# Performance work log

Hardware: AMD Instinct MI355X
Metric: run time of the kernel (lower is better)

Reference implementation:

```python
import jax, jax.numpy as jnp
import numpy as np

B, C, Q, E, H = 8, 1024, 128, 512, 1024


def setup_inputs() -> dict:
    key = jax.random.key(0)
    ks = jax.random.split(key, 8)
    return {
        "context": jax.random.normal(ks[0], (B, C, E), jnp.float32),
        "question": jax.random.normal(ks[1], (B, Q, E), jnp.float32),
        "context_mask": jnp.ones((B, C), jnp.float32),
        "w_question": jax.random.normal(ks[2], (E,), jnp.float32),
        "w_context": jax.random.normal(ks[3], (E,), jnp.float32),
        "w_multiple": jax.random.normal(ks[4], (E,), jnp.float32),
        "W1": jax.random.normal(ks[5], (4 * E, H), jnp.float32) * 0.02,
        "b1": jnp.zeros((H,), jnp.float32),
        "W2": jax.random.normal(ks[6], (H, 4 * E), jnp.float32) * 0.02,
        "b2": jnp.zeros((4 * E,), jnp.float32),
    }


def reference(context, question, context_mask, w_question, w_context, w_multiple, W1, b1, W2, b2):
    # Dropout is identity at eval time.
    # Trilinear similarity: s[b,c,q] = q.w_q + ctx.w_c + sum_e q_e*ctx_e*w_m_e
    q_w = question @ w_question                                  # (B,Q)
    c_w = context @ w_context                                    # (B,C)
    mult = jnp.einsum("bqe,bce->bcq", question * w_multiple, context)  # avoids (B,C,Q,E)
    sim = q_w[:, None, :] + c_w[:, :, None] + mult               # (B,C,Q)

    # Context2Query: softmax over question dim (dim=2)
    c2q = jnp.einsum("bcq,bqe->bce", jax.nn.softmax(sim, axis=2), question)
    # Query2Context: max over question dim, softmax over context dim (dim=1)
    q2c = jnp.einsum("bc,bce->be", jax.nn.softmax(jnp.max(sim, axis=2), axis=1), context)  # (B,E)

    attended = jnp.concatenate(
        [context, c2q, context * c2q, context * q2c[:, None, :]], axis=2
    )  # (B,C,4E)

    # MaskedLinear: linear then zero out masked context positions
    m = context_mask[:, :, None]
    h = (attended @ W1 + b1) * m
    out = jax.nn.relu((h @ W2 + b2) * m)
    return out
```

## Files before the change

### kernel.cpp

```cpp
#include <hip/hip_runtime.h>

typedef __bf16 bf16;
typedef __bf16 bf16x2 __attribute__((ext_vector_type(2)));
typedef __bf16 bf16x4 __attribute__((ext_vector_type(4)));
typedef __bf16 bf16x8 __attribute__((ext_vector_type(8)));
typedef float f32x4 __attribute__((ext_vector_type(4)));

#define AS1 __attribute__((address_space(1)))
#define AS3 __attribute__((address_space(3)))

__device__ __forceinline__ void async_copy16(const void* g, void* l) {
  __builtin_amdgcn_global_load_lds((const AS1 void*)g, (AS3 void*)l, 16, 0, 0);
}

#define BB 8
#define CC 1024
#define QQ 128
#define EE 512
#define HH 1024
#define FOURE 2048

__global__ __launch_bounds__(256) void prep_kernel(
    const float* __restrict__ W1, const float* __restrict__ W2,
    const float* __restrict__ qst, const float* __restrict__ wmul,
    const float* __restrict__ wqv, bf16* __restrict__ W1T,
    bf16* __restrict__ W2T, bf16* __restrict__ qT,
    bf16* __restrict__ qmh, bf16* __restrict__ qml, float* __restrict__ qw) {
  __shared__ float tile[32][33];
  __shared__ float r4[4];
  int bx = blockIdx.x;
  int t = threadIdx.x;
  if (bx >= 4608) {
    int i = bx - 4608;
    int half = t >> 7, tr = t & 127;
    int rowg = i * 2 + half;
    const float* qrow = qst + (size_t)rowg * EE;
    float4 qv = *(const float4*)&qrow[tr * 4];
    float4 wm4 = *(const float4*)&wmul[tr * 4];
    float4 wq4 = *(const float4*)&wqv[tr * 4];
    float m[4] = {qv.x * wm4.x, qv.y * wm4.y, qv.z * wm4.z, qv.w * wm4.w};
    bf16x4 h, l;
#pragma unroll
    for (int k = 0; k < 4; ++k) {
      bf16 hh = (bf16)m[k];
      h[k] = hh; l[k] = (bf16)(m[k] - (float)hh);
    }
    *(bf16x4*)&qmh[(size_t)rowg * EE + tr * 4] = h;
    *(bf16x4*)&qml[(size_t)rowg * EE + tr * 4] = l;
    float s = qv.x * wq4.x + qv.y * wq4.y + qv.z * wq4.z + qv.w * wq4.w;
#pragma unroll
    for (int off = 32; off; off >>= 1) s += __shfl_xor(s, off);
    if ((t & 63) == 0) r4[t >> 6] = s;
    __syncthreads();
    if (tr == 0) qw[rowg] = r4[half * 2] + r4[half * 2 + 1];
    return;
  }
  const float* src;
  bf16* dst;
  int R, C, idx;
  if (bx < 2048) {
    src = W1; dst = W1T; R = 2048; C = 1024; idx = bx;
  } else if (bx < 4096) {
    src = W2; dst = W2T; R = 1024; C = 2048; idx = bx - 2048;
  } else {
    int i = bx - 4096;
    int b = i >> 6; idx = i & 63;
    src = qst + (size_t)b * QQ * EE; dst = qT + (size_t)b * EE * QQ;
    R = 128; C = 512;
  }
  int ctiles = C >> 5;
  int by = idx / ctiles, cx = idx % ctiles;
  int tx = t & 31, ty = t >> 5;
#pragma unroll
  for (int rr = 0; rr < 4; ++rr)
    tile[ty + rr * 8][tx] = src[(size_t)(by * 32 + ty + rr * 8) * C + cx * 32 + tx];
  __syncthreads();
#pragma unroll
  for (int rr = 0; rr < 4; ++rr)
    dst[(size_t)(cx * 32 + ty + rr * 8) * R + by * 32 + tx] = (bf16)tile[tx][ty + rr * 8];
}

__global__ __launch_bounds__(256) void fused_att_kernel(
    const float* __restrict__ ctx, const bf16* __restrict__ qmh,
    const bf16* __restrict__ qml, const bf16* __restrict__ qT,
    const float* __restrict__ wc, const float* __restrict__ qw,
    float* __restrict__ smax, bf16* __restrict__ att) {
  int b = blockIdx.y;
  int m0 = blockIdx.x * 16;
  __shared__ __align__(16) char U[26880];
  bf16* Ah = (bf16*)(U);
  bf16* Al = (bf16*)(U + 1024);
  bf16* Bh = (bf16*)(U + 2048);
  bf16* Bl = (bf16*)(U + 10240);
  float(*sim_s)[132] = (float(*)[132])(U + 18432);
  bf16* c2q_lds = (bf16*)(U);
  __shared__ float wc_s[EE];
  __shared__ float qw_s[QQ];
  __shared__ float cw_s[16];
  __shared__ bf16 P_lds[16][136];
  int t = threadIdx.x;
  for (int i = t; i < EE; i += 256) wc_s[i] = wc[i];
  if (t < QQ) qw_s[t] = qw[b * QQ + t];
  __syncthreads();
  int wv = t >> 6, ln = t & 63;
  int rl = ln & 15, kq = ln >> 4;
  f32x4 acc[2] = {};
  const float* Ag = ctx + ((size_t)b * CC + m0) * EE;
  const bf16* Bhg = qmh + (size_t)b * QQ * EE;
  const bf16* Blg = qml + (size_t)b * QQ * EE;
  int arow = t >> 4, ae = (t & 15) * 2;
  float cwp = 0.f;
  for (int k0 = 0; k0 < EE; k0 += 32) {
    {
      float2 v = *(const float2*)(Ag + (size_t)arow * EE + k0 + ae);
      cwp += v.x * wc_s[k0 + ae] + v.y * wc_s[k0 + ae + 1];
      bf16 h0 = (bf16)v.x, h1 = (bf16)v.y;
      bf16x2 h, l;
      h[0] = h0; h[1] = h1;
      l[0] = (bf16)(v.x - (float)h0);
      l[1] = (bf16)(v.y - (float)h1);
      int sl = ((ae >> 3) ^ ((arow >> 1) & 3)) * 8 + (ae & 7);
      *(bf16x2*)&Ah[arow * 32 + sl] = h;
      *(bf16x2*)&Al[arow * 32 + sl] = l;
    }
#pragma unroll
    for (int r = 0; r < 2; ++r) {
      int fb = (r * 4 + wv) * 1024 + ln * 16;
      int row = fb >> 6;
      int cq = ((fb >> 4) & 3) ^ ((row >> 1) & 3);
      async_copy16(Bhg + (size_t)row * EE + k0 + cq * 8, (char*)Bh + fb);
      async_copy16(Blg + (size_t)row * EE + k0 + cq * 8, (char*)Bl + fb);
    }
    __syncthreads();
    bf16x8 ah, al, bh[2], bl[2];
    {
      int sl = (kq ^ ((rl >> 1) & 3)) * 8;
      ah = *(const bf16x8*)&Ah[rl * 32 + sl];
      al = *(const bf16x8*)&Al[rl * 32 + sl];
    }
#pragma unroll
    for (int j = 0; j < 2; ++j) {
      int r = wv * 32 + j * 16 + rl;
      int sl = (kq ^ ((r >> 1) & 3)) * 8;
      bh[j] = *(const bf16x8*)&Bh[r * 32 + sl];
      bl[j] = *(const bf16x8*)&Bl[r * 32 + sl];
    }
#pragma unroll
    for (int j = 0; j < 2; ++j) {
      acc[j] = __builtin_amdgcn_mfma_f32_16x16x32_bf16(ah, bh[j], acc[j], 0, 0, 0);
      acc[j] = __builtin_amdgcn_mfma_f32_16x16x32_bf16(ah, bl[j], acc[j], 0, 0, 0);
      acc[j] = __builtin_amdgcn_mfma_f32_16x16x32_bf16(al, bh[j], acc[j], 0, 0, 0);
    }
    __syncthreads();
  }
  {
    float s = cwp;
    s += __shfl_xor(s, 1); s += __shfl_xor(s, 2);
    s += __shfl_xor(s, 4); s += __shfl_xor(s, 8);
    if ((t & 15) == 0) cw_s[arow] = s;
  }
#pragma unroll
  for (int j = 0; j < 2; ++j) {
    int col = wv * 32 + j * 16 + rl;
    float qv = qw_s[col];
    int rbase = kq * 4;
#pragma unroll
    for (int r = 0; r < 4; ++r) sim_s[rbase + r][col] = acc[j][r] + qv;
  }
  __syncthreads();
  {
    int row = t >> 4, cb = t & 15;
    float v[8];
    float mx = -3.4e38f;
#pragma unroll
    for (int k = 0; k < 8; ++k) {
      v[k] = sim_s[row][cb + 16 * k];
      mx = fmaxf(mx, v[k]);
    }
    mx = fmaxf(mx, __shfl_xor(mx, 1));
    mx = fmaxf(mx, __shfl_xor(mx, 2));
    mx = fmaxf(mx, __shfl_xor(mx, 4));
    mx = fmaxf(mx, __shfl_xor(mx, 8));
    float sm = 0.f;
#pragma unroll
    for (int k = 0; k < 8; ++k) { v[k] = __expf(v[k] - mx); sm += v[k]; }
    sm += __shfl_xor(sm, 1);
    sm += __shfl_xor(sm, 2);
    sm += __shfl_xor(sm, 4);
    sm += __shfl_xor(sm, 8);
    float inv = 1.0f / sm;
#pragma unroll
    for (int k = 0; k < 8; ++k) P_lds[row][cb + 16 * k] = (bf16)(v[k] * inv);
    if (cb == 0) smax[b * CC + m0 + row] = mx + cw_s[row];
  }
  __syncthreads();
  f32x4 acc2[8] = {};
  const bf16* qTb = qT + (size_t)b * EE * QQ;
#pragma unroll
  for (int kk = 0; kk < 4; ++kk) {
    bf16x8 af2;
    {
      bf16x4 lo = *(const bf16x4*)&P_lds[rl][kk * 32 + kq * 8];
      bf16x4 hi = *(const bf16x4*)&P_lds[rl][kk * 32 + kq * 8 + 4];
      af2[0] = lo[0]; af2[1] = lo[1]; af2[2] = lo[2]; af2[3] = lo[3];
      af2[4] = hi[0]; af2[5] = hi[1]; af2[6] = hi[2]; af2[7] = hi[3];
    }
#pragma unroll
    for (int j = 0; j < 8; ++j) {
      int n = wv * 128 + j * 16 + rl;
      bf16x8 bfr = *(const bf16x8*)&qTb[(size_t)n * QQ + kk * 32 + kq * 8];
      acc2[j] = __builtin_amdgcn_mfma_f32_16x16x32_bf16(af2, bfr, acc2[j], 0, 0, 0);
    }
  }
#pragma unroll
  for (int j = 0; j < 8; ++j) {
    int col = wv * 128 + j * 16 + rl;
    int rbase = kq * 4;
#pragma unroll
    for (int r = 0; r < 4; ++r)
      c2q_lds[(size_t)(rbase + r) * 520 + col] = (bf16)acc2[j][r];
  }
  __syncthreads();
  {
    int row = t >> 4, tc = t & 15;
    const float* crow = ctx + ((size_t)(b * CC + m0 + row)) * EE;
    bf16* arow_p = att + ((size_t)(b * CC + m0 + row)) * FOURE;
#pragma unroll
    for (int cc = 0; cc < 4; ++cc) {
      int col = cc * 128 + tc * 8;
      bf16x8 q8 = *(const bf16x8*)&c2q_lds[(size_t)row * 520 + col];
      float4 v0 = *(const float4*)&crow[col];
      float4 v1 = *(const float4*)&crow[col + 4];
      float cv[8] = {v0.x, v0.y, v0.z, v0.w, v1.x, v1.y, v1.z, v1.w};
      bf16x8 o0, o2;
#pragma unroll
      for (int k = 0; k < 8; ++k) {
        o0[k] = (bf16)cv[k];
        o2[k] = (bf16)(cv[k] * (float)q8[k]);
      }
      *(bf16x8*)&arow_p[col] = o0;
      *(bf16x8*)&arow_p[EE + col] = q8;
      *(bf16x8*)&arow_p[2 * EE + col] = o2;
    }
  }
}

__global__ __launch_bounds__(256) void q2c_kernel(
    const float* __restrict__ ctx, const float* __restrict__ smax,
    float* __restrict__ q2c) {
  int b = blockIdx.x >> 5, ch = blockIdx.x & 31;
  int t = threadIdx.x;
  __shared__ float red[256];
  __shared__ float w_s[32];
  float v[4];
  float mx = -3.4e38f;
#pragma unroll
  for (int i = 0; i < 4; ++i) {
    v[i] = smax[b * CC + i * 256 + t];
    mx = fmaxf(mx, v[i]);
  }
  red[t] = mx;
  __syncthreads();
  for (int s = 128; s > 0; s >>= 1) {
    if (t < s) red[t] = fmaxf(red[t], red[t + s]);
    __syncthreads();
  }
  mx = red[0];
  __syncthreads();
  float sm = 0.f;
#pragma unroll
  for (int i = 0; i < 4; ++i) sm += __expf(v[i] - mx);
  red[t] = sm;
  __syncthreads();
  for (int s = 128; s > 0; s >>= 1) {
    if (t < s) red[t] += red[t + s];
    __syncthreads();
  }
  float inv = 1.0f / red[0];
  if (t < 32) w_s[t] = __expf(smax[b * CC + ch * 32 + t] - mx) * inv;
  __syncthreads();
  int e = t * 2;
  const float* cb = ctx + ((size_t)b * CC + ch * 32) * EE;
  float a0 = 0.f, a1 = 0.f;
#pragma unroll 8
  for (int r = 0; r < 32; ++r) {
    float2 vv = *(const float2*)&cb[(size_t)r * EE + e];
    float w = w_s[r];
    a0 += w * vv.x;
    a1 += w * vv.y;
  }
  atomicAdd(&q2c[b * EE + e], a0);
  atomicAdd(&q2c[b * EE + e + 1], a1);
}

__global__ __launch_bounds__(256) void att3_kernel(
    const float* __restrict__ ctx, const float* __restrict__ q2c,
    bf16* __restrict__ att) {
  int idx = blockIdx.x * 256 + threadIdx.x;
  int row = idx >> 6;
  int e = (idx & 63) * 8;
  int b = row >> 10;
  float4 v0 = *(const float4*)&ctx[(size_t)row * EE + e];
  float4 v1 = *(const float4*)&ctx[(size_t)row * EE + e + 4];
  float4 g0 = *(const float4*)&q2c[b * EE + e];
  float4 g1 = *(const float4*)&q2c[b * EE + e + 4];
  bf16x8 o;
  o[0] = (bf16)(v0.x * g0.x); o[1] = (bf16)(v0.y * g0.y);
  o[2] = (bf16)(v0.z * g0.z); o[3] = (bf16)(v0.w * g0.w);
  o[4] = (bf16)(v1.x * g1.x); o[5] = (bf16)(v1.y * g1.y);
  o[6] = (bf16)(v1.z * g1.z); o[7] = (bf16)(v1.w * g1.w);
  *(bf16x8*)&att[(size_t)row * FOURE + 3 * EE + e] = o;
}

template <int OUT_BF16, int RELU>
__global__ __launch_bounds__(512, 2) void gemm_bt_db_kernel(
    const bf16* __restrict__ A, const bf16* __restrict__ Bt,
    const float* __restrict__ bias, const float* __restrict__ mask,
    void* __restrict__ Cout, int M, int N, int K) {
  __shared__ bf16 As[3][128 * 64];
  __shared__ bf16 Bs[3][256 * 64];
  int ntn = N >> 8;
  int nblk = (M >> 7) * ntn;
  int cpx = nblk >> 3;
  int bid = blockIdx.x;
  int swz = (bid & 7) * cpx + (bid >> 3);
  int mt = swz / ntn, ntb = swz - mt * ntn;
  int m0 = mt << 7, n0 = ntb << 8;
  int t = threadIdx.x, wv = t >> 6, ln = t & 63;
  int wm = wv >> 2, wn = wv & 3;
  int rl = ln & 15, kq = ln >> 4;
  int NT = K >> 6;

  auto stage = [&](int buf, int kt) {
    int k0 = kt << 6;
#pragma unroll
    for (int r = 0; r < 2; ++r) {
      int fb = r * 8192 + t * 16;
      int row = fb >> 7;
      int q = ((fb >> 4) & 7) ^ (row & 7);
      async_copy16(A + (size_t)(m0 + row) * K + k0 + q * 8,
                   (char*)As[buf] + fb);
    }
#pragma unroll
    for (int r = 0; r < 4; ++r) {
      int fb = r * 8192 + t * 16;
      int row = fb >> 7;
      int q = ((fb >> 4) & 7) ^ (row & 7);
      async_copy16(Bt + (size_t)(n0 + row) * K + k0 + q * 8,
                   (char*)Bs[buf] + fb);
    }
  };

  stage(0, 0);
  stage(1, 1);
  asm volatile("s_waitcnt vmcnt(6)" ::: "memory");
  __builtin_amdgcn_s_barrier();
  asm volatile("" ::: "memory");

  f32x4 acc[4][4] = {};
  int cur = 0, nx2 = 2;
  for (int tt = 0; tt < NT; ++tt) {
    if (tt + 2 < NT) stage(nx2, tt + 2);
    const bf16* Ab = As[cur];
    const bf16* Bb = Bs[cur];
#pragma unroll
    for (int ks = 0; ks < 2; ++ks) {
      int c = ks * 4 + kq;
      bf16x8 af[4], bfr[4];
#pragma unroll
      for (int i = 0; i < 4; ++i) {
        int row = wm * 64 + i * 16 + rl;
        af[i] = *(const bf16x8*)&Ab[row * 64 + ((c ^ (row & 7)) * 8)];
      }
#pragma unroll
      for (int j = 0; j < 4; ++j) {
        int row = wn * 64 + j * 16 + rl;
        bfr[j] = *(const bf16x8*)&Bb[row * 64 + ((c ^ (row & 7)) * 8)];
      }
#pragma unroll
      for (int i = 0; i < 4; ++i)
#pragma unroll
        for (int j = 0; j < 4; ++j)
          acc[i][j] = __builtin_amdgcn_mfma_f32_16x16x32_bf16(
              af[i], bfr[j], acc[i][j], 0, 0, 0);
    }
    if (tt + 1 < NT) {
      if (tt + 2 < NT)
        asm volatile("s_waitcnt vmcnt(6)" ::: "memory");
      else
        asm volatile("s_waitcnt vmcnt(0)" ::: "memory");
      __builtin_amdgcn_s_barrier();
      asm volatile("" ::: "memory");
    }
    cur = cur == 2 ? 0 : cur + 1;
    nx2 = nx2 == 2 ? 0 : nx2 + 1;
  }

#pragma unroll
  for (int j = 0; j < 4; ++j) {
    int col = n0 + wn * 64 + j * 16 + rl;
    float bv = bias[col];
#pragma unroll
    for (int i = 0; i < 4; ++i) {
      int rbase = m0 + wm * 64 + i * 16 + (kq << 2);
#pragma unroll
      for (int r = 0; r < 4; ++r) {
        int row = rbase + r;
        float v = acc[i][j][r] + bv;
        v *= mask[row];
        if (RELU) v = fmaxf(v, 0.f);
        if (OUT_BF16)
          ((bf16*)Cout)[(size_t)row * N + col] = (bf16)v;
        else
          ((float*)Cout)[(size_t)row * N + col] = v;
      }
    }
  }
}

extern "C" void kernel_launch(void* const* d_in, const int* in_sizes, int n_in,
                              void* d_out, int out_size, void* d_ws, size_t ws_size,
                              hipStream_t stream) {
  const float* ctx = (const float*)d_in[0];
  const float* qst = (const float*)d_in[1];
  const float* mask = (const float*)d_in[2];
  const float* wqv = (const float*)d_in[3];
  const float* wcv = (const float*)d_in[4];
  const float* wmul = (const float*)d_in[5];
  const float* W1 = (const float*)d_in[6];
  const float* b1 = (const float*)d_in[7];
  const float* W2 = (const float*)d_in[8];
  const float* b2 = (const float*)d_in[9];
  float* out = (float*)d_out;
  char* ws = (char*)d_ws;

  bf16* att = (bf16*)(ws);
  bf16* hbuf = (bf16*)(ws + 33554432);
  bf16* W1T = (bf16*)(ws + 50331648);
  bf16* W2T = (bf16*)(ws + 54525952);
  bf16* qT = (bf16*)(ws + 58720256);
  bf16* qmh = (bf16*)(ws + 59768832);
  bf16* qml = (bf16*)(ws + 60817408);
  float* smax = (float*)(ws + 61865984);
  float* q2c = (float*)(ws + 61898752);
  float* qw = (float*)(ws + 61915136);

  prep_kernel<<<5120, 256, 0, stream>>>(W1, W2, qst, wmul, wqv,
                                        W1T, W2T, qT, qmh, qml, qw);
  fused_att_kernel<<<dim3(64, BB), 256, 0, stream>>>(ctx, qmh, qml, qT, wcv,
                                                     qw, smax, att);
  hipMemsetAsync(q2c, 0, BB * EE * sizeof(float), stream);
  q2c_kernel<<<256, 256, 0, stream>>>(ctx, smax, q2c);
  att3_kernel<<<2048, 256, 0, stream>>>(ctx, q2c, att);
  gemm_bt_db_kernel<1, 0><<<256, 512, 0, stream>>>(
      att, W1T, b1, mask, hbuf, 8192, 1024, 2048);
  gemm_bt_db_kernel<0, 1><<<512, 512, 0, stream>>>(
      hbuf, W2T, b2, mask, out, 8192, 2048, 1024);
}
```

Measured before the change: 238.5 us.

## Restructure bf16 GEMM into 256x128 tiles with split-phase prefetch and MFMA priority

The two MLP GEMMs now use 256x128 block tiles with a 4x2 wave layout and a grouped block-to-tile mapping, in place of 128x256 tiles with an XCD-strided swizzle. Each K step is split into two halves. Each half reads its LDS fragments, issues part of the next-next stage's async global-to-LDS loads, and then runs its MFMAs at raised wave priority. The aim is to interleave global loads, LDS reads and matrix work across waves so more latency is hidden. The cost is more barriers per K iteration and a different L2 reuse pattern from the new tile order.

```diff
diff --git a/kernel.cpp b/kernel.cpp
--- a/kernel.cpp
+++ b/kernel.cpp
@@ -313,87 +313,115 @@
 }
 
 template <int OUT_BF16, int RELU>
-__global__ __launch_bounds__(512, 2) void gemm_bt_db_kernel(
+__global__ __launch_bounds__(512, 2) void gemm_bt_p2_kernel(
     const bf16* __restrict__ A, const bf16* __restrict__ Bt,
     const float* __restrict__ bias, const float* __restrict__ mask,
     void* __restrict__ Cout, int M, int N, int K) {
-  __shared__ bf16 As[3][128 * 64];
-  __shared__ bf16 Bs[3][256 * 64];
-  int ntn = N >> 8;
-  int nblk = (M >> 7) * ntn;
-  int cpx = nblk >> 3;
-  int bid = blockIdx.x;
-  int swz = (bid & 7) * cpx + (bid >> 3);
-  int mt = swz / ntn, ntb = swz - mt * ntn;
-  int m0 = mt << 7, n0 = ntb << 8;
+  __shared__ bf16 As[3][256 * 64];
+  __shared__ bf16 Bs[3][128 * 64];
+  int ntiles = N >> 7;
+  int tiles_per_g = 8 * ntiles;
+  int g = blockIdx.x / tiles_per_g, sub = blockIdx.x % tiles_per_g;
+  int mt = g * 8 + (sub & 7), ntb = sub >> 3;
+  int m0 = mt << 8, n0 = ntb << 7;
   int t = threadIdx.x, wv = t >> 6, ln = t & 63;
-  int wm = wv >> 2, wn = wv & 3;
+  int wm = wv >> 1, wn = wv & 1;
   int rl = ln & 15, kq = ln >> 4;
   int NT = K >> 6;
 
-  auto stage = [&](int buf, int kt) {
+  auto stageA = [&](int buf, int kt, int r) {
     int k0 = kt << 6;
-#pragma unroll
-    for (int r = 0; r < 2; ++r) {
-      int fb = r * 8192 + t * 16;
-      int row = fb >> 7;
-      int q = ((fb >> 4) & 7) ^ (row & 7);
-      async_copy16(A + (size_t)(m0 + row) * K + k0 + q * 8,
-                   (char*)As[buf] + fb);
-    }
-#pragma unroll
-    for (int r = 0; r < 4; ++r) {
-      int fb = r * 8192 + t * 16;
-      int row = fb >> 7;
-      int q = ((fb >> 4) & 7) ^ (row & 7);
-      async_copy16(Bt + (size_t)(n0 + row) * K + k0 + q * 8,
-                   (char*)Bs[buf] + fb);
-    }
+    int fb = r * 8192 + t * 16;
+    int row = fb >> 7;
+    int q = ((fb >> 4) & 7) ^ (row & 7);
+    async_copy16(A + (size_t)(m0 + row) * K + k0 + q * 8, (char*)As[buf] + fb);
   };
-
-  stage(0, 0);
-  stage(1, 1);
+  auto stageB = [&](int buf, int kt, int r) {
+    int k0 = kt << 6;
+    int fb = r * 8192 + t * 16;
+    int row = fb >> 7;
+    int q = ((fb >> 4) & 7) ^ (row & 7);
+    async_copy16(Bt + (size_t)(n0 + row) * K + k0 + q * 8, (char*)Bs[buf] + fb);
+  };
+
+#pragma unroll
+  for (int r = 0; r < 4; ++r) stageA(0, 0, r);
+#pragma unroll
+  for (int r = 0; r < 2; ++r) stageB(0, 0, r);
+#pragma unroll
+  for (int r = 0; r < 4; ++r) stageA(1, 1, r);
+#pragma unroll
+  for (int r = 0; r < 2; ++r) stageB(1, 1, r);
   asm volatile("s_waitcnt vmcnt(6)" ::: "memory");
   __builtin_amdgcn_s_barrier();
-  asm volatile("" ::: "memory");
 
   f32x4 acc[4][4] = {};
-  int cur = 0, nx2 = 2;
-  for (int tt = 0; tt < NT; ++tt) {
-    if (tt + 2 < NT) stage(nx2, tt + 2);
+  int cur = 0;
+  for (int kt = 0; kt < NT; ++kt) {
     const bf16* Ab = As[cur];
     const bf16* Bb = Bs[cur];
+    int nxt = cur + 2; if (nxt >= 3) nxt -= 3;
+    bool pf = (kt + 2) < NT;
+    bf16x8 af0[2][2], bfr[2][4];
 #pragma unroll
     for (int ks = 0; ks < 2; ++ks) {
       int c = ks * 4 + kq;
-      bf16x8 af[4], bfr[4];
-#pragma unroll
-      for (int i = 0; i < 4; ++i) {
+#pragma unroll
+      for (int i = 0; i < 2; ++i) {
         int row = wm * 64 + i * 16 + rl;
-        af[i] = *(const bf16x8*)&Ab[row * 64 + ((c ^ (row & 7)) * 8)];
+        af0[ks][i] = *(const bf16x8*)&Ab[row * 64 + ((c ^ (row & 7)) * 8)];
       }
 #pragma unroll
       for (int j = 0; j < 4; ++j) {
         int row = wn * 64 + j * 16 + rl;
-        bfr[j] = *(const bf16x8*)&Bb[row * 64 + ((c ^ (row & 7)) * 8)];
+        bfr[ks][j] = *(const bf16x8*)&Bb[row * 64 + ((c ^ (row & 7)) * 8)];
       }
-#pragma unroll
-      for (int i = 0; i < 4; ++i)
+    }
+    if (pf) { stageA(nxt, kt + 2, 0); stageA(nxt, kt + 2, 1); stageA(nxt, kt + 2, 2); }
+    __builtin_amdgcn_s_barrier();
+    asm volatile("s_waitcnt lgkmcnt(0)" ::: "memory");
+    __builtin_amdgcn_sched_barrier(0);
+    __builtin_amdgcn_s_setprio(1);
+#pragma unroll
+    for (int ks = 0; ks < 2; ++ks)
+#pragma unroll
+      for (int i = 0; i < 2; ++i)
 #pragma unroll
         for (int j = 0; j < 4; ++j)
           acc[i][j] = __builtin_amdgcn_mfma_f32_16x16x32_bf16(
-              af[i], bfr[j], acc[i][j], 0, 0, 0);
-    }
-    if (tt + 1 < NT) {
-      if (tt + 2 < NT)
-        asm volatile("s_waitcnt vmcnt(6)" ::: "memory");
-      else
-        asm volatile("s_waitcnt vmcnt(0)" ::: "memory");
+              af0[ks][i], bfr[ks][j], acc[i][j], 0, 0, 0);
+    __builtin_amdgcn_s_setprio(0);
+    __builtin_amdgcn_s_barrier();
+    bf16x8 af1[2][2];
+#pragma unroll
+    for (int ks = 0; ks < 2; ++ks) {
+      int c = ks * 4 + kq;
+#pragma unroll
+      for (int i = 0; i < 2; ++i) {
+        int row = wm * 64 + (i + 2) * 16 + rl;
+        af1[ks][i] = *(const bf16x8*)&Ab[row * 64 + ((c ^ (row & 7)) * 8)];
+      }
+    }
+    if (pf) { stageA(nxt, kt + 2, 3); stageB(nxt, kt + 2, 0); stageB(nxt, kt + 2, 1); }
+    __builtin_amdgcn_s_barrier();
+    asm volatile("s_waitcnt lgkmcnt(0)" ::: "memory");
+    __builtin_amdgcn_sched_barrier(0);
+    __builtin_amdgcn_s_setprio(1);
+#pragma unroll
+    for (int ks = 0; ks < 2; ++ks)
+#pragma unroll
+      for (int i = 0; i < 2; ++i)
+#pragma unroll
+        for (int j = 0; j < 4; ++j)
+          acc[i + 2][j] = __builtin_amdgcn_mfma_f32_16x16x32_bf16(
+              af1[ks][i], bfr[ks][j], acc[i + 2][j], 0, 0, 0);
+    __builtin_amdgcn_s_setprio(0);
+    if (kt + 1 < NT) {
+      if (pf) asm volatile("s_waitcnt vmcnt(6)" ::: "memory");
+      else    asm volatile("s_waitcnt vmcnt(0)" ::: "memory");
       __builtin_amdgcn_s_barrier();
-      asm volatile("" ::: "memory");
-    }
-    cur = cur == 2 ? 0 : cur + 1;
-    nx2 = nx2 == 2 ? 0 : nx2 + 1;
+    }
+    cur += 1; if (cur >= 3) cur -= 3;
   }
 
 #pragma unroll
@@ -452,8 +480,8 @@
   hipMemsetAsync(q2c, 0, BB * EE * sizeof(float), stream);
   q2c_kernel<<<256, 256, 0, stream>>>(ctx, smax, q2c);
   att3_kernel<<<2048, 256, 0, stream>>>(ctx, q2c, att);
-  gemm_bt_db_kernel<1, 0><<<256, 512, 0, stream>>>(
+  gemm_bt_p2_kernel<1, 0><<<256, 512, 0, stream>>>(
       att, W1T, b1, mask, hbuf, 8192, 1024, 2048);
-  gemm_bt_db_kernel<0, 1><<<512, 512, 0, stream>>>(
+  gemm_bt_p2_kernel<0, 1><<<512, 512, 0, stream>>>(
       hbuf, W2T, b2, mask, out, 8192, 2048, 1024);
 }
```

Result: faster. 224.9 us (-5.7%).
